# Optimization experiments

Measured on AMD Instinct MI355X. Metric: run time of the kernel, lower is better.

The kernel has to match this reference:

```python
import jax, jax.numpy as jnp
import numpy as np

B, C, D, H = 32, 512, 512, 8  # batch, enc_in channels, d_model, num_heads
W = D // H                    # per-head width in frequency domain
BN_EPS = 1e-5


def _lin(k, din, dout):
    # weight stored as [in, out]; apply as x @ W + b (equivalent to torch Linear)
    return jax.random.normal(k, (din, dout), jnp.float32) / np.sqrt(din)


def setup_inputs() -> dict:
    key = jax.random.key(0)
    ks = jax.random.split(key, 16)
    return {
        "x": jax.random.normal(ks[0], (B, C, D), jnp.float32),
        "W_in": _lin(ks[1], D, D), "b_in": jnp.zeros((D,), jnp.float32),
        "W_q": _lin(ks[2], D, D), "b_q": jnp.zeros((D,), jnp.float32),
        "W_k": _lin(ks[3], D, D), "b_k": jnp.zeros((D,), jnp.float32),
        "W_v": _lin(ks[4], D, D), "b_v": jnp.zeros((D,), jnp.float32),
        "temperature": jnp.ones((H, 1), jnp.float32),
        "W1a": _lin(ks[5], D, D), "b1a": jnp.zeros((D,), jnp.float32),
        "bn_gamma": jnp.ones((C,), jnp.float32),
        "bn_beta": jnp.zeros((C,), jnp.float32),
        "bn_mean": 0.1 * jax.random.normal(ks[6], (C,), jnp.float32),
        "bn_var": 1.0 + 0.1 * jax.random.uniform(ks[7], (C,), jnp.float32),
        "W1b": _lin(ks[8], D, D), "b1b": jnp.zeros((D,), jnp.float32),
        "W_out": _lin(ks[9], 2 * D, D), "b_out": jnp.zeros((D,), jnp.float32),
    }


def _complex_l2_normalize(z):
    # torch F.normalize on complex: divide by L2 norm of |z| along last dim
    n = jnp.sqrt(jnp.sum(jnp.abs(z) ** 2, axis=-1, keepdims=True))
    return z / jnp.maximum(n, 1e-12)


def reference(x, W_in, b_in, W_q, b_q, W_k, b_k, W_v, b_v, temperature,
              W1a, b1a, bn_gamma, bn_beta, bn_mean, bn_var, W1b, b1b,
              W_out, b_out):
    b, c, d = x.shape
    h, w = H, d // H

    conv2 = x @ W_in + b_in                       # in_projector (dropout = identity, eval)
    q = conv2 @ W_q + b_q
    k = conv2 @ W_k + b_k
    v = conv2 @ W_v + b_v

    # 2-D FFT over last two axes (c, d), as torch.fft.fft2 does on [b, c, d]
    q_f = jnp.fft.fft2(q).reshape(b, c, h, w)
    k_f = jnp.fft.fft2(k).reshape(b, c, h, w)
    v_f = jnp.fft.fft2(v).reshape(b, c, h, w)
    tep = jnp.fft.fft2(conv2)                     # [b, c, d] complex

    q_f = _complex_l2_normalize(q_f)
    k_f = _complex_l2_normalize(k_f)

    # [b, c, h, h] complex attention scores, scaled by real (8,1) temperature
    attn = jnp.einsum('bchw,bcgw->bchg', q_f, k_f) * temperature
    # custom complex softmax: softmax real and imag parts independently
    attn = jax.nn.softmax(attn.real, axis=-1) + 1j * jax.nn.softmax(attn.imag, axis=-1)

    out_f = jnp.einsum('bchg,bcgw->bchw', attn, v_f)        # complex [b,c,h,w]
    out_f = jnp.abs(jnp.fft.ifft2(out_f)).reshape(b, c, d)  # ifft2 over (h,w)

    # gated branch: Linear -> BatchNorm1d(enc_in, eval) -> ReLU -> Linear -> Sigmoid
    g = tep.real @ W1a + b1a
    g = (g - bn_mean[None, :, None]) * jax.lax.rsqrt(bn_var[None, :, None] + BN_EPS)
    g = g * bn_gamma[None, :, None] + bn_beta[None, :, None]
    g = jax.nn.relu(g) @ W1b + b1b
    g = jax.nn.sigmoid(g)
    out_l = jnp.abs(jnp.fft.ifft2(g * tep))                 # [b, c, d]

    out2 = jnp.concatenate([out_f, out_l], axis=-1) @ W_out + b_out
    return out2 + conv2
```

## Files before the change

### kernel.cpp

```cpp
#include <hip/hip_runtime.h>
#include <hip/hip_bf16.h>

#define FFT_PI 3.14159265358979323846f
#define FOFF(i) ((i) + ((i) >> 3))
#define PR(r) ((r) ^ (((r) >> 3) & 1))

typedef __hip_bfloat16 bf16;
typedef short bf8_t __attribute__((ext_vector_type(8)));
typedef float f4_t __attribute__((ext_vector_type(4)));

__device__ inline float bf2f(unsigned short u) {
    union { unsigned int i; float f; } v; v.i = ((unsigned int)u) << 16; return v.f;
}
__device__ inline unsigned short f2bf(float f) {
    bf16 h = __float2bfloat16(f);
    union { bf16 h; unsigned short u; } v; v.h = h; return v.u;
}
__device__ inline float2 c_load(const ushort2* p) {
    ushort2 u = *p;
    return make_float2(bf2f(u.x), bf2f(u.y));
}
__device__ inline ushort2 c_store(float2 z) {
    ushort2 u; u.x = f2bf(z.x); u.y = f2bf(z.y); return u;
}
__device__ inline int brev6(int t) {
    return ((t & 1) << 5) | ((t & 2) << 3) | ((t & 4) << 1) |
           ((t & 8) >> 1) | ((t & 16) >> 3) | ((t & 32) >> 5);
}
__device__ inline float2 cadd(float2 a, float2 b){ return make_float2(a.x+b.x, a.y+b.y); }
__device__ inline float2 csub(float2 a, float2 b){ return make_float2(a.x-b.x, a.y-b.y); }
__device__ inline float2 cmul(float2 a, float2 b){
    return make_float2(a.x*b.x - a.y*b.y, a.x*b.y + a.y*b.x);
}
__device__ inline float2 cmuli(float2 a, float s){ return make_float2(-s*a.y, s*a.x); }

__device__ inline float2 twd(const float2* TWL, int j, float sign) {
    float2 t = TWL[j];
    return make_float2(t.x, sign * t.y);
}

__device__ inline void async_load16(const void* gp, void* lp) {
    __builtin_amdgcn_global_load_lds(
        (const __attribute__((address_space(1))) void*)gp,
        (__attribute__((address_space(3))) void*)lp, 16, 0, 0);
}

__global__ __launch_bounds__(256) void transpose_cvt_all(
    const float* __restrict__ s0, const float* __restrict__ s1,
    const float* __restrict__ s2, const float* __restrict__ s3,
    const float* __restrict__ s4, const float* __restrict__ s5,
    const float* __restrict__ s6, bf16* __restrict__ Wt)
{
    const int z = blockIdx.z;
    const int R = (z == 6) ? 1024 : 512;
    if (blockIdx.y * 32 >= R) return;
    const float* src = (z == 0) ? s0 : (z == 1) ? s1 : (z == 2) ? s2 :
                       (z == 3) ? s3 : (z == 4) ? s4 : (z == 5) ? s5 : s6;
    bf16* dst = Wt + (long)z * 262144;
    const int C = 512;

    __shared__ float tile[32][33];
    const int bx = blockIdx.x * 32;
    const int by = blockIdx.y * 32;
    const int tx = threadIdx.x, ty = threadIdx.y;
#pragma unroll
    for (int i = 0; i < 32; i += 8)
        tile[ty + i][tx] = src[(long)(by + ty + i) * C + bx + tx];
    __syncthreads();
#pragma unroll
    for (int i = 0; i < 32; i += 8)
        dst[(long)(bx + ty + i) * R + by + tx] = __float2bfloat16(tile[tx][ty + i]);
}

__global__ __launch_bounds__(256) void mfma_gemm(
    const void* __restrict__ Av, const void* __restrict__ Av2,
    int a_type, int lda, int ksplit,
    const bf16* __restrict__ Bt, int ldb,
    const float* __restrict__ bias0, const float* __restrict__ bias1,
    const float* __restrict__ bias2,
    void* __restrict__ C0, void* __restrict__ C1, void* __restrict__ C2,
    int nper, int out_type, int ldc, int K,
    const float* __restrict__ e0, const float* __restrict__ e1,
    const float* __restrict__ e2, const float* __restrict__ e3)
{
    __shared__ short Asub[128 * 32];
    __shared__ short Bsub[128 * 32];

    const int tid = threadIdx.x;
    const int n0 = blockIdx.x * 128;
    const int m0 = blockIdx.y * 128;
    const int l  = tid & 63;
    const int wv = tid >> 6;
    const int wm = wv & 1, wn = wv >> 1;

    f4_t acc[4][4];
#pragma unroll
    for (int i = 0; i < 4; i++)
#pragma unroll
        for (int j = 0; j < 4; j++)
            acc[i][j] = (f4_t)0.f;

    const int crow = l >> 2;
    const int cpc  = (l & 3) * 8;

    for (int k0 = 0; k0 < K; k0 += 32) {
        const void* As = (k0 < ksplit) ? Av : Av2;
        const int kk = (k0 < ksplit) ? k0 : (k0 - ksplit);

        if (a_type == 0) {
#pragma unroll
            for (int c = 0; c < 2; c++) {
                const int chunk = wv * 2 + c;
                const int row = chunk * 16 + crow;
                async_load16((const bf16*)As + (long)(m0 + row) * lda + kk + cpc,
                             &Asub[chunk * 512]);
                async_load16(Bt + (long)(n0 + row) * ldb + k0 + cpc,
                             &Bsub[chunk * 512]);
            }
        } else {
            const int srow = tid >> 2;
            const int sc8  = (tid & 3) * 8;
#pragma unroll
            for (int p = 0; p < 2; p++) {
                const int row = srow + p * 64;
                const float4* src = (const float4*)((const float*)As
                    + (long)(m0 + row) * lda + kk + sc8);
                float4 u0 = src[0], u1 = src[1];
                bf8_t av;
                av[0] = (short)f2bf(u0.x); av[1] = (short)f2bf(u0.y);
                av[2] = (short)f2bf(u0.z); av[3] = (short)f2bf(u0.w);
                av[4] = (short)f2bf(u1.x); av[5] = (short)f2bf(u1.y);
                av[6] = (short)f2bf(u1.z); av[7] = (short)f2bf(u1.w);
                *(bf8_t*)&Asub[row * 32 + sc8] = av;
            }
#pragma unroll
            for (int c = 0; c < 2; c++) {
                const int chunk = wv * 2 + c;
                const int row = chunk * 16 + crow;
                async_load16(Bt + (long)(n0 + row) * ldb + k0 + cpc,
                             &Bsub[chunk * 512]);
            }
        }
        __syncthreads();

        bf8_t a_frag[4], b_frag[4];
        const int ko = (l >> 4) * 8;
        const int lr = l & 15;
#pragma unroll
        for (int fm = 0; fm < 4; fm++)
            a_frag[fm] = *(bf8_t*)&Asub[(wm * 64 + fm * 16 + lr) * 32 + ko];
#pragma unroll
        for (int fn = 0; fn < 4; fn++)
            b_frag[fn] = *(bf8_t*)&Bsub[(wn * 64 + fn * 16 + lr) * 32 + ko];
#pragma unroll
        for (int fm = 0; fm < 4; fm++)
#pragma unroll
            for (int fn = 0; fn < 4; fn++)
                acc[fm][fn] = __builtin_amdgcn_mfma_f32_16x16x32_bf16(
                    b_frag[fn], a_frag[fm], acc[fm][fn], 0, 0, 0);
        __syncthreads();
    }

    const int sel = n0 / nper;
    const int nb  = sel * nper;
    const float* biasl = (sel == 0) ? bias0 : ((sel == 1) ? bias1 : bias2);
    void* Cl = (sel == 0) ? C0 : ((sel == 1) ? C1 : C2);

    const int em = m0 + wm * 64 + (l & 15);
    const int en = n0 + wn * 64 + ((l >> 4) << 2);
#pragma unroll
    for (int fm = 0; fm < 4; fm++) {
        const long m = em + fm * 16;
        float bnm = 0.f, bnr = 1.f, bng = 1.f, bnb = 0.f;
        if (out_type == 3) {
            const int c = (int)(m & 511);
            bnm = e0[c];
            bnr = 1.0f / sqrtf(e1[c] + 1e-5f);
            bng = e2[c];
            bnb = e3[c];
        }
#pragma unroll
        for (int fn = 0; fn < 4; fn++) {
            const int n = en + fn * 16;
            const int nl = n - nb;
            f4_t v = acc[fm][fn];
            if (biasl) {
#pragma unroll
                for (int r = 0; r < 4; r++) v[r] += biasl[nl + r];
            }
            if (out_type == 0) {
                float4 o; o.x = v[0]; o.y = v[1]; o.z = v[2]; o.w = v[3];
                *(float4*)((float*)Cl + m * ldc + nl) = o;
            } else if (out_type == 1) {
                union { unsigned short u[4]; ushort4 q; } o;
#pragma unroll
                for (int r = 0; r < 4; r++) o.u[r] = f2bf(v[r]);
                *(ushort4*)((bf16*)Cl + m * ldc + nl) = o.q;
            } else if (out_type == 2) {
                union { ushort2 u2[4]; uint4 q; } o;
#pragma unroll
                for (int r = 0; r < 4; r++) { o.u2[r].x = f2bf(v[r]); o.u2[r].y = 0; }
                *(uint4*)((ushort2*)Cl + m * ldc + nl) = o.q;
            } else if (out_type == 3) {
                union { unsigned short u[4]; ushort4 q; } o;
#pragma unroll
                for (int r = 0; r < 4; r++)
                    o.u[r] = f2bf(fmaxf((v[r] - bnm) * bnr * bng + bnb, 0.f));
                *(ushort4*)((bf16*)Cl + m * ldc + nl) = o.q;
            } else {
                union { unsigned short u[4]; ushort4 q; } rsd;
                rsd.q = *(const ushort4*)((const unsigned short*)e0 + m * ldc + nl);
                float4 o;
                o.x = v[0] + bf2f(rsd.u[0]);
                o.y = v[1] + bf2f(rsd.u[1]);
                o.z = v[2] + bf2f(rsd.u[2]);
                o.w = v[3] + bf2f(rsd.u[3]);
                *(float4*)((float*)Cl + m * ldc + nl) = o;
            }
        }
    }
}

__device__ inline void dft8(float2* x, float sgn)
{
    const float c45 = 0.70710678118654752f;
    float2 e0, e1, e2, e3, o0, o1, o2, o3;
    {
        float2 u0 = cadd(x[0], x[4]), u1 = csub(x[0], x[4]);
        float2 u2 = cadd(x[2], x[6]), u3 = cmuli(csub(x[2], x[6]), sgn);
        e0 = cadd(u0, u2); e1 = cadd(u1, u3); e2 = csub(u0, u2); e3 = csub(u1, u3);
    }
    {
        float2 u0 = cadd(x[1], x[5]), u1 = csub(x[1], x[5]);
        float2 u2 = cadd(x[3], x[7]), u3 = cmuli(csub(x[3], x[7]), sgn);
        o0 = cadd(u0, u2); o1 = cadd(u1, u3); o2 = csub(u0, u2); o3 = csub(u1, u3);
    }
    const float2 w1 = make_float2(c45, sgn * c45);
    const float2 w3 = make_float2(-c45, sgn * c45);
    o1 = cmul(o1, w1);
    o2 = cmuli(o2, sgn);
    o3 = cmul(o3, w3);
    x[0] = cadd(e0, o0); x[4] = csub(e0, o0);
    x[1] = cadd(e1, o1); x[5] = csub(e1, o1);
    x[2] = cadd(e2, o2); x[6] = csub(e2, o2);
    x[3] = cadd(e3, o3); x[7] = csub(e3, o3);
}

__device__ inline void fft512_r8u(ushort2* bx0, ushort2* by0, int lane, float sign,
                                  const float2* TWL)
{
    ushort2* bx = bx0;
    ushort2* by = by0;
#pragma unroll
    for (int st = 0; st < 3; st++) {
        int n, m, sstr, p, q;
        if (st == 0)      { n = 512; m = 64; sstr = 1;  p = lane;      q = 0; }
        else if (st == 1) { n = 64;  m = 8;  sstr = 8;  p = lane >> 3; q = lane & 7; }
        else              { n = 8;   m = 1;  sstr = 64; p = 0;         q = lane; }
        float2 x[8];
#pragma unroll
        for (int r = 0; r < 8; r++) x[r] = c_load(&bx[FOFF(q + sstr * (p + r * m))]);
        dft8(x, sign);
        if (p) {
            const int step = (st == 0) ? 1 : 8;
#pragma unroll
            for (int k = 1; k < 8; k++)
                x[k] = cmul(x[k], twd(TWL, p * k * step, sign));
        }
#pragma unroll
        for (int k = 0; k < 8; k++) by[FOFF(q + sstr * (8 * p + k))] = c_store(x[k]);
        ushort2* t = bx; bx = by; by = t;
    }
}

__device__ inline void twl_fill(float2* TWL, int t, int nthreads)
{
    for (int j = t; j < 512; j += nthreads) {
        float sw, cw;
        __sincosf((2.0f * FFT_PI) * (float)j / 512.0f, &sw, &cw);
        TWL[j] = make_float2(cw, sw);
    }
}

__global__ __launch_bounds__(256) void fft8_rows_all(
    ushort2* __restrict__ qkv, const bf16* __restrict__ conv2,
    ushort2* __restrict__ tb)
{
    __shared__ ushort2 B0[4][576], B1[4][576];
    __shared__ float2 TWL[512];
    const int buf = blockIdx.x >> 12;
    const int lb  = blockIdx.x & 4095;
    const int li = threadIdx.x >> 6, lane = threadIdx.x & 63;
    const long line = (long)lb * 4 + li;
    twl_fill(TWL, threadIdx.x, 256);

    if (buf < 3) {
        ushort2* s = qkv + (long)buf * 8388608 + line * 512;
        uint4 r0 = *(const uint4*)(s + lane * 8);
        uint4 r1 = *(const uint4*)(s + lane * 8 + 4);
        ushort2* dst = &B0[li][9 * lane];
        const ushort2* pp = (const ushort2*)&r0;
#pragma unroll
        for (int j = 0; j < 4; j++) dst[j] = pp[j];
        pp = (const ushort2*)&r1;
#pragma unroll
        for (int j = 0; j < 4; j++) dst[4 + j] = pp[j];
        __syncthreads();
        fft512_r8u(B0[li], B1[li], lane, -1.f, TWL);
        ushort2* src = &B1[li][9 * lane];
        union { ushort2 u[4]; uint4 q; } o0, o1;
#pragma unroll
        for (int j = 0; j < 4; j++) o0.u[j] = src[j];
#pragma unroll
        for (int j = 0; j < 4; j++) o1.u[j] = src[4 + j];
        *(uint4*)(s + lane * 8) = o0.q;
        *(uint4*)(s + lane * 8 + 4) = o1.q;
    } else {
        uint4 raw = *(const uint4*)((const unsigned short*)conv2 + line * 512 + lane * 8);
        const unsigned short* pp = (const unsigned short*)&raw;
        ushort2* d = &B0[li][9 * lane];
#pragma unroll
        for (int j = 0; j < 8; j++) { ushort2 u; u.x = pp[j]; u.y = 0; d[j] = u; }
        __syncthreads();
        fft512_r8u(B0[li], B1[li], lane, -1.f, TWL);
        ushort2* s = tb + line * 512;
        ushort2* src = &B1[li][9 * lane];
        union { ushort2 u[4]; uint4 q; } o0, o1;
#pragma unroll
        for (int j = 0; j < 4; j++) o0.u[j] = src[j];
#pragma unroll
        for (int j = 0; j < 4; j++) o1.u[j] = src[4 + j];
        *(uint4*)(s + lane * 8) = o0.q;
        *(uint4*)(s + lane * 8 + 4) = o1.q;
    }
}

__global__ __launch_bounds__(256) void fft8_rows_gated(
    const bf16* __restrict__ g2, ushort2* __restrict__ tep)
{
    __shared__ ushort2 B0[4][576], B1[4][576];
    __shared__ float2 TWL[512];
    const int li = threadIdx.x >> 6, lane = threadIdx.x & 63;
    const long line = (long)blockIdx.x * 4 + li;
    ushort2* s = tep + line * 512;
    twl_fill(TWL, threadIdx.x, 256);
    {
        uint4 rg = *(const uint4*)((const unsigned short*)g2 + line * 512 + lane * 8);
        uint4 r0 = *(const uint4*)(s + lane * 8);
        uint4 r1 = *(const uint4*)(s + lane * 8 + 4);
        const unsigned short* gp = (const unsigned short*)&rg;
        ushort2* d = &B0[li][9 * lane];
        const ushort2* pp = (const ushort2*)&r0;
#pragma unroll
        for (int j = 0; j < 4; j++) {
            float sg = 1.0f / (1.0f + __expf(-bf2f(gp[j])));
            float2 z = c_load(pp + j);
            d[j] = c_store(make_float2(sg * z.x, sg * z.y));
        }
        pp = (const ushort2*)&r1;
#pragma unroll
        for (int j = 0; j < 4; j++) {
            float sg = 1.0f / (1.0f + __expf(-bf2f(gp[4 + j])));
            float2 z = c_load(pp + j);
            d[4 + j] = c_store(make_float2(sg * z.x, sg * z.y));
        }
    }
    __syncthreads();
    fft512_r8u(B0[li], B1[li], lane, +1.f, TWL);
    {
        const float sc = 1.0f / 512.0f;
        ushort2* src = &B1[li][9 * lane];
        union { ushort2 u[4]; uint4 q; } o0, o1;
#pragma unroll
        for (int j = 0; j < 4; j++) {
            float2 z = c_load(&src[j]);
            o0.u[j] = c_store(make_float2(z.x * sc, z.y * sc));
        }
#pragma unroll
        for (int j = 0; j < 4; j++) {
            float2 z = c_load(&src[4 + j]);
            o1.u[j] = c_store(make_float2(z.x * sc, z.y * sc));
        }
        *(uint4*)(s + lane * 8) = o0.q;
        *(uint4*)(s + lane * 8 + 4) = o1.q;
    }
}

__global__ __launch_bounds__(512) void fft8_cols16_c2c4(
    ushort2* __restrict__ data, bf16* __restrict__ tepReal, float sign)
{
    __shared__ __align__(16) ushort2 Bu[512][16];
    __shared__ float2 TWL[512];
    const int buf = blockIdx.x >> 10;
    const int rem = blockIdx.x & 1023;
    const int b   = rem >> 5;
    const int c0  = (rem & 31) * 16;
    ushort2* base = data + (long)buf * 8388608 + (long)b * 262144 + c0;
    const int t = threadIdx.x;
    const int lr = t >> 2;
    const int lq = t & 3;
    twl_fill(TWL, t, 512);

#pragma unroll
    for (int it = 0; it < 4; it++) {
        const int row = it * 128 + lr;
        uint4 raw = *(const uint4*)(base + (long)row * 512 + lq * 4);
        *(uint4*)&Bu[PR(row)][lq * 4] = raw;
    }
    __syncthreads();

    const int col = t & 15;
    const int rb  = t >> 4;
#pragma unroll
    for (int st = 0; st < 3; st++) {
        int n, m, s;
        if (st == 0)      { n = 512; m = 64; s = 1;  }
        else if (st == 1) { n = 64;  m = 8;  s = 8;  }
        else              { n = 8;   m = 1;  s = 64; }
        const int step = (st == 0) ? 1 : 8;
        float2 x[2][8];
        int ps[2], qs[2];
#pragma unroll
        for (int i = 0; i < 2; i++) {
            const int role = rb + 32 * i;
            int p, q;
            if (st == 0)      { p = role;      q = 0; }
            else if (st == 1) { p = role >> 3; q = role & 7; }
            else              { p = 0;         q = role; }
            ps[i] = p; qs[i] = q;
#pragma unroll
            for (int r = 0; r < 8; r++) {
                const int rr = q + s * (p + r * m);
                x[i][r] = c_load(&Bu[PR(rr)][col]);
            }
        }
        __syncthreads();
#pragma unroll
        for (int i = 0; i < 2; i++) {
            dft8(x[i], sign);
            const int p = ps[i];
            if (p) {
#pragma unroll
                for (int k = 1; k < 8; k++)
                    x[i][k] = cmul(x[i][k], twd(TWL, p * k * step, sign));
            }
#pragma unroll
            for (int k = 0; k < 8; k++) {
                const int rw = qs[i] + s * (8 * p + k);
                Bu[PR(rw)][col] = c_store(x[i][k]);
            }
        }
        __syncthreads();
    }

#pragma unroll
    for (int it = 0; it < 4; it++) {
        const int row = it * 128 + lr;
        union { uint4 q4; unsigned short s[8]; } o;
        o.q4 = *(const uint4*)&Bu[PR(row)][lq * 4];
        *(uint4*)(base + (long)row * 512 + lq * 4) = o.q4;
        if (buf == 3) {
            ushort4 rl;
            rl.x = o.s[0]; rl.y = o.s[2]; rl.z = o.s[4]; rl.w = o.s[6];
            *(ushort4*)(tepReal + (long)b * 262144 + (long)row * 512 + c0 + lq * 4) = rl;
        }
    }
}

__global__ __launch_bounds__(512) void fft8_cols16_abs(
    const ushort2* __restrict__ src, bf16* __restrict__ dst)
{
    __shared__ __align__(16) ushort2 Bu[512][16];
    __shared__ float2 TWL[512];
    const int b  = blockIdx.x >> 5;
    const int c0 = (blockIdx.x & 31) * 16;
    const ushort2* base = src + (long)b * 262144 + c0;
    const int t = threadIdx.x;
    const int lr = t >> 2;
    const int lq = t & 3;
    twl_fill(TWL, t, 512);

#pragma unroll
    for (int it = 0; it < 4; it++) {
        const int row = it * 128 + lr;
        uint4 raw = *(const uint4*)(base + (long)row * 512 + lq * 4);
        *(uint4*)&Bu[PR(row)][lq * 4] = raw;
    }
    __syncthreads();

    const int col = t & 15;
    const int rb  = t >> 4;
#pragma unroll
    for (int st = 0; st < 3; st++) {
        int n, m, s;
        if (st == 0)      { n = 512; m = 64; s = 1;  }
        else if (st == 1) { n = 64;  m = 8;  s = 8;  }
        else              { n = 8;   m = 1;  s = 64; }
        const int step = (st == 0) ? 1 : 8;
        float2 x[2][8];
        int ps[2], qs[2];
#pragma unroll
        for (int i = 0; i < 2; i++) {
            const int role = rb + 32 * i;
            int p, q;
            if (st == 0)      { p = role;      q = 0; }
            else if (st == 1) { p = role >> 3; q = role & 7; }
            else              { p = 0;         q = role; }
            ps[i] = p; qs[i] = q;
#pragma unroll
            for (int r = 0; r < 8; r++) {
                const int rr = q + s * (p + r * m);
                x[i][r] = c_load(&Bu[PR(rr)][col]);
            }
        }
        __syncthreads();
#pragma unroll
        for (int i = 0; i < 2; i++) {
            dft8(x[i], +1.f);
            const int p = ps[i];
            if (p) {
#pragma unroll
                for (int k = 1; k < 8; k++)
                    x[i][k] = cmul(x[i][k], twd(TWL, p * k * step, +1.f));
            }
#pragma unroll
            for (int k = 0; k < 8; k++) {
                const int rw = qs[i] + s * (8 * p + k);
                Bu[PR(rw)][col] = c_store(x[i][k]);
            }
        }
        __syncthreads();
    }

    const float sc = 1.0f / 512.0f;
#pragma unroll
    for (int it = 0; it < 4; it++) {
        const int row = it * 128 + lr;
        union { unsigned short u[4]; ushort4 q4; } o;
#pragma unroll
        for (int j = 0; j < 4; j++) {
            float2 z = c_load(&Bu[PR(row)][lq * 4 + j]);
            o.u[j] = f2bf(sqrtf(z.x * z.x + z.y * z.y) * sc);
        }
        *(ushort4*)(dst + (long)b * 262144 + (long)row * 512 + c0 + lq * 4) = o.q4;
    }
}

__global__ __launch_bounds__(256) void attn_kernel(
    const ushort2* __restrict__ qf, const ushort2* __restrict__ kf,
    const ushort2* __restrict__ vf, const float* __restrict__ temp,
    bf16* __restrict__ out_f)
{
    __shared__ ushort2 QS[4][8][68];
    __shared__ ushort2 KS[4][8][68];
    __shared__ float2 ATT[4][8][9];
    __shared__ float2 TW32[32];

    const int li = threadIdx.x >> 6, lane = threadIdx.x & 63;
    const int bc = blockIdx.x * 4 + li;
    const long base = (long)bc * 512;

    if (lane < 32) {
        float sw, cw;
        __sincosf((FFT_PI / 32.0f) * (float)lane, &sw, &cw);
        TW32[lane] = make_float2(cw, sw);
    }

    {
        const int h1 = lane >> 4, w1 = (lane & 15) * 4;
        uint4 q0 = *(const uint4*)(qf + base + lane * 4);
        uint4 q1 = *(const uint4*)(qf + base + 256 + lane * 4);
        uint4 k0 = *(const uint4*)(kf + base + lane * 4);
        uint4 k1 = *(const uint4*)(kf + base + 256 + lane * 4);
        *(uint4*)&QS[li][h1][w1]     = q0;
        *(uint4*)&QS[li][h1 + 4][w1] = q1;
        *(uint4*)&KS[li][h1][w1]     = k0;
        *(uint4*)&KS[li][h1 + 4][w1] = k1;
    }
    float2 v[8];
#pragma unroll
    for (int h = 0; h < 8; h++)
        v[h] = c_load(vf + base + h * 64 + lane);

    {
        const int h = lane >> 3, g = lane & 7;
        float ar = 0.f, ai = 0.f, nq = 0.f, nk = 0.f;
#pragma unroll
        for (int w = 0; w < 64; w += 4) {
            uint4 qa = *(const uint4*)&QS[li][h][w];
            uint4 kb = *(const uint4*)&KS[li][g][w];
            const unsigned short* qs = (const unsigned short*)&qa;
            const unsigned short* ks = (const unsigned short*)&kb;
#pragma unroll
            for (int j = 0; j < 4; j++) {
                float qx = bf2f(qs[2 * j]), qy = bf2f(qs[2 * j + 1]);
                float kx = bf2f(ks[2 * j]), ky = bf2f(ks[2 * j + 1]);
                ar += qx * kx - qy * ky;
                ai += qx * ky + qy * kx;
                nq += qx * qx + qy * qy;
                nk += kx * kx + ky * ky;
            }
        }
        const float iq = 1.0f / fmaxf(sqrtf(nq), 1e-12f);
        const float ik = 1.0f / fmaxf(sqrtf(nk), 1e-12f);
        const float s = temp[h] * iq * ik;
        ar *= s; ai *= s;
        float mr = ar, mi = ai;
#pragma unroll
        for (int o = 1; o < 8; o <<= 1) {
            mr = fmaxf(mr, __shfl_xor(mr, o, 64));
            mi = fmaxf(mi, __shfl_xor(mi, o, 64));
        }
        float er = __expf(ar - mr), ei = __expf(ai - mi);
        float sr = er, si = ei;
#pragma unroll
        for (int o = 1; o < 8; o <<= 1) {
            sr += __shfl_xor(sr, o, 64);
            si += __shfl_xor(si, o, 64);
        }
        ATT[li][h][g] = make_float2(er / sr, ei / si);
    }

    float2 o[8];
#pragma unroll
    for (int h = 0; h < 8; h++) {
        float orr = 0.f, oi = 0.f;
#pragma unroll
        for (int g = 0; g < 8; g++) {
            float2 a = ATT[li][h][g], b = v[g];
            orr += a.x * b.x - a.y * b.y;
            oi  += a.x * b.y + a.y * b.x;
        }
        o[h] = make_float2(orr, oi);
    }

#pragma unroll
    for (int m = 32; m >= 1; m >>= 1) {
        const int j = (lane & (m - 1)) * (32 / m);
        float2 wv = TW32[j];
        const float cw = wv.x, sw = wv.y;
        const bool low = (lane & m) == 0;
#pragma unroll
        for (int h = 0; h < 8; h++) {
            float px = __shfl_xor(o[h].x, m, 64);
            float py = __shfl_xor(o[h].y, m, 64);
            float nx, ny;
            if (low) {
                nx = o[h].x + px;
                ny = o[h].y + py;
            } else {
                float dx = px - o[h].x;
                float dy = py - o[h].y;
                nx = dx * cw - dy * sw;
                ny = dx * sw + dy * cw;
            }
            o[h].x = nx; o[h].y = ny;
        }
    }
    const int wr = brev6(lane);

    const float r2 = 0.70710678118654752f;
    const float W8x[8] = {1.f,  r2, 0.f, -r2, -1.f, -r2,  0.f,  r2};
    const float W8y[8] = {0.f,  r2, 1.f,  r2,  0.f, -r2, -1.f, -r2};
    unsigned short* stg = (unsigned short*)&QS[li][0][0];
#pragma unroll
    for (int kh = 0; kh < 8; kh++) {
        float sr = 0.f, si = 0.f;
#pragma unroll
        for (int n = 0; n < 8; n++) {
            const int idx = (n * kh) & 7;
            float wx = W8x[idx], wy = W8y[idx];
            sr += o[n].x * wx - o[n].y * wy;
            si += o[n].x * wy + o[n].y * wx;
        }
        stg[kh * 64 + wr] = f2bf(sqrtf(sr * sr + si * si) * (1.0f / 512.0f));
    }
    uint4 ov = *(uint4*)(stg + lane * 8);
    *(uint4*)((unsigned short*)out_f + base + lane * 8) = ov;
}

extern "C" void kernel_launch(void* const* d_in, const int* in_sizes, int n_in,
                              void* d_out, int out_size, void* d_ws, size_t ws_size,
                              hipStream_t stream)
{
    const float* x     = (const float*)d_in[0];
    const float* W_in  = (const float*)d_in[1];
    const float* b_in  = (const float*)d_in[2];
    const float* W_q   = (const float*)d_in[3];
    const float* b_q   = (const float*)d_in[4];
    const float* W_k   = (const float*)d_in[5];
    const float* b_k   = (const float*)d_in[6];
    const float* W_v   = (const float*)d_in[7];
    const float* b_v   = (const float*)d_in[8];
    const float* temp  = (const float*)d_in[9];
    const float* W1a   = (const float*)d_in[10];
    const float* b1a   = (const float*)d_in[11];
    const float* gam   = (const float*)d_in[12];
    const float* bet   = (const float*)d_in[13];
    const float* mea   = (const float*)d_in[14];
    const float* var   = (const float*)d_in[15];
    const float* W1b   = (const float*)d_in[16];
    const float* b1b   = (const float*)d_in[17];
    const float* W_out = (const float*)d_in[18];
    const float* b_out = (const float*)d_in[19];

    char* wsb = (char*)d_ws;
    const long MB = 1024 * 1024;
    bf16*    conv2b  = (bf16*)wsb;
    bf16*    tepReal = (bf16*)(wsb + 16 * MB);
    ushort2* Qb    = (ushort2*)(wsb + 32 * MB);
    ushort2* Kb    = (ushort2*)(wsb + 64 * MB);
    ushort2* Vb    = (ushort2*)(wsb + 96 * MB);
    ushort2* Tb    = (ushort2*)(wsb + 128 * MB);
    bf16*    Wt    = (bf16*)(wsb + 160 * MB);
    bf16* WT_in  = Wt;
    bf16* WT_q   = Wt + 262144;
    bf16* WT_1a  = Wt + 4 * 262144;
    bf16* WT_1b  = Wt + 5 * 262144;
    bf16* WT_out = Wt + 6 * 262144;
    bf16* outF = (bf16*)Qb;
    bf16* g1b  = (bf16*)Kb;
    bf16* outL = (bf16*)Kb;
    bf16* g2b  = (bf16*)Vb;

    const dim3 ggrid(4, 128), gblk(256);
    const int BIG = 1 << 30;
    const int RB = 4096;

    transpose_cvt_all<<<dim3(16, 32, 7), dim3(32, 8), 0, stream>>>(
        W_in, W_q, W_k, W_v, W1a, W1b, W_out, Wt);

    mfma_gemm<<<ggrid, gblk, 0, stream>>>(
        x, x, 1, 512, BIG, WT_in, 512, b_in, nullptr, nullptr,
        conv2b, nullptr, nullptr, BIG, 1, 512, 512,
        nullptr, nullptr, nullptr, nullptr);

    mfma_gemm<<<dim3(12, 128), gblk, 0, stream>>>(
        conv2b, conv2b, 0, 512, BIG, WT_q, 512, b_q, b_k, b_v,
        Qb, Kb, Vb, 512, 2, 512, 512,
        nullptr, nullptr, nullptr, nullptr);

    fft8_rows_all<<<4 * RB, 256, 0, stream>>>(Qb, conv2b, Tb);

    fft8_cols16_c2c4<<<4096, 512, 0, stream>>>(Qb, tepReal, -1.f);

    attn_kernel<<<RB, 256, 0, stream>>>(Qb, Kb, Vb, temp, outF);

    mfma_gemm<<<ggrid, gblk, 0, stream>>>(
        tepReal, tepReal, 0, 512, BIG, WT_1a, 512, b1a, nullptr, nullptr,
        g1b, nullptr, nullptr, BIG, 3, 512, 512,
        mea, var, gam, bet);

    mfma_gemm<<<ggrid, gblk, 0, stream>>>(
        g1b, g1b, 0, 512, BIG, WT_1b, 512, b1b, nullptr, nullptr,
        g2b, nullptr, nullptr, BIG, 1, 512, 512,
        nullptr, nullptr, nullptr, nullptr);

    fft8_rows_gated<<<RB, 256, 0, stream>>>(g2b, Tb);
    fft8_cols16_abs<<<1024, 512, 0, stream>>>(Tb, outL);

    mfma_gemm<<<ggrid, gblk, 0, stream>>>(
        outF, outL, 0, 512, 512, WT_out, 1024, b_out, nullptr, nullptr,
        d_out, nullptr, nullptr, BIG, 4, 512, 1024,
        (const float*)conv2b, nullptr, nullptr, nullptr);
}
```

Baseline: 519.8 us.

## Co-schedule attention blocks with gated-branch GEMMs and row FFT in fused launches

The attention kernel is split into three slices, and each slice is merged into the same launch as one gated-branch stage: the two GEMMs and the gated row FFT. Blocks are dispatched by block index to either body and share a union of shared memory. The aim is to let the independent attention work and the memory-heavy gated work overlap on the GPU and fill idle CUs. The gated intermediates move into the output buffer to avoid aliasing with Kb/Vb, which attention still reads. The cost is that the shared-memory union takes the larger of the two sizes, and register usage is now that of the heavier body, which may lower occupancy.

```diff
diff --git a/kernel.cpp b/kernel.cpp
--- a/kernel.cpp
+++ b/kernel.cpp
@@ -44,6 +44,22 @@
         (const __attribute__((address_space(1))) void*)gp,
         (__attribute__((address_space(3))) void*)lp, 16, 0, 0);
 }
+
+struct AttnSmem {
+    ushort2 QS[4][8][68];
+    ushort2 KS[4][8][68];
+    float2  ATT[4][8][9];
+    float2  TW32[32];
+};
+struct GemmSmem {
+    short Asub[128 * 32];
+    short Bsub[128 * 32];
+};
+struct RowsSmem {
+    ushort2 B0[4][576];
+    ushort2 B1[4][576];
+    float2  TWL[512];
+};
 
 __global__ __launch_bounds__(256) void transpose_cvt_all(
     const float* __restrict__ s0, const float* __restrict__ s1,
@@ -72,7 +88,7 @@
         dst[(long)(bx + ty + i) * R + by + tx] = __float2bfloat16(tile[tx][ty + i]);
 }
 
-__global__ __launch_bounds__(256) void mfma_gemm(
+__device__ void gemm_body(GemmSmem& sm, int bx, int by,
     const void* __restrict__ Av, const void* __restrict__ Av2,
     int a_type, int lda, int ksplit,
     const bf16* __restrict__ Bt, int ldb,
@@ -83,12 +99,12 @@
     const float* __restrict__ e0, const float* __restrict__ e1,
     const float* __restrict__ e2, const float* __restrict__ e3)
 {
-    __shared__ short Asub[128 * 32];
-    __shared__ short Bsub[128 * 32];
+    short* Asub = sm.Asub;
+    short* Bsub = sm.Bsub;
 
     const int tid = threadIdx.x;
-    const int n0 = blockIdx.x * 128;
-    const int m0 = blockIdx.y * 128;
+    const int n0 = bx * 128;
+    const int m0 = by * 128;
     const int l  = tid & 63;
     const int wv = tid >> 6;
     const int wm = wv & 1, wn = wv >> 1;
@@ -221,6 +237,23 @@
     }
 }
 
+__global__ __launch_bounds__(256) void mfma_gemm(
+    const void* __restrict__ Av, const void* __restrict__ Av2,
+    int a_type, int lda, int ksplit,
+    const bf16* __restrict__ Bt, int ldb,
+    const float* __restrict__ bias0, const float* __restrict__ bias1,
+    const float* __restrict__ bias2,
+    void* __restrict__ C0, void* __restrict__ C1, void* __restrict__ C2,
+    int nper, int out_type, int ldc, int K,
+    const float* __restrict__ e0, const float* __restrict__ e1,
+    const float* __restrict__ e2, const float* __restrict__ e3)
+{
+    __shared__ GemmSmem sm;
+    gemm_body(sm, blockIdx.x, blockIdx.y, Av, Av2, a_type, lda, ksplit,
+              Bt, ldb, bias0, bias1, bias2, C0, C1, C2,
+              nper, out_type, ldc, K, e0, e1, e2, e3);
+}
+
 __device__ inline void dft8(float2* x, float sgn)
 {
     const float c45 = 0.70710678118654752f;
@@ -335,21 +368,19 @@
     }
 }
 
-__global__ __launch_bounds__(256) void fft8_rows_gated(
+__device__ void rows_gated_body(RowsSmem& sm, int blk,
     const bf16* __restrict__ g2, ushort2* __restrict__ tep)
 {
-    __shared__ ushort2 B0[4][576], B1[4][576];
-    __shared__ float2 TWL[512];
     const int li = threadIdx.x >> 6, lane = threadIdx.x & 63;
-    const long line = (long)blockIdx.x * 4 + li;
+    const long line = (long)blk * 4 + li;
     ushort2* s = tep + line * 512;
-    twl_fill(TWL, threadIdx.x, 256);
+    twl_fill(sm.TWL, threadIdx.x, 256);
     {
         uint4 rg = *(const uint4*)((const unsigned short*)g2 + line * 512 + lane * 8);
         uint4 r0 = *(const uint4*)(s + lane * 8);
         uint4 r1 = *(const uint4*)(s + lane * 8 + 4);
         const unsigned short* gp = (const unsigned short*)&rg;
-        ushort2* d = &B0[li][9 * lane];
+        ushort2* d = &sm.B0[li][9 * lane];
         const ushort2* pp = (const ushort2*)&r0;
 #pragma unroll
         for (int j = 0; j < 4; j++) {
@@ -366,10 +397,10 @@
         }
     }
     __syncthreads();
-    fft512_r8u(B0[li], B1[li], lane, +1.f, TWL);
+    fft512_r8u(sm.B0[li], sm.B1[li], lane, +1.f, sm.TWL);
     {
         const float sc = 1.0f / 512.0f;
-        ushort2* src = &B1[li][9 * lane];
+        ushort2* src = &sm.B1[li][9 * lane];
         union { ushort2 u[4]; uint4 q; } o0, o1;
 #pragma unroll
         for (int j = 0; j < 4; j++) {
@@ -546,24 +577,19 @@
     }
 }
 
-__global__ __launch_bounds__(256) void attn_kernel(
+__device__ void attn_body(AttnSmem& sm, int blk,
     const ushort2* __restrict__ qf, const ushort2* __restrict__ kf,
     const ushort2* __restrict__ vf, const float* __restrict__ temp,
     bf16* __restrict__ out_f)
 {
-    __shared__ ushort2 QS[4][8][68];
-    __shared__ ushort2 KS[4][8][68];
-    __shared__ float2 ATT[4][8][9];
-    __shared__ float2 TW32[32];
-
     const int li = threadIdx.x >> 6, lane = threadIdx.x & 63;
-    const int bc = blockIdx.x * 4 + li;
+    const int bc = blk * 4 + li;
     const long base = (long)bc * 512;
 
     if (lane < 32) {
         float sw, cw;
         __sincosf((FFT_PI / 32.0f) * (float)lane, &sw, &cw);
-        TW32[lane] = make_float2(cw, sw);
+        sm.TW32[lane] = make_float2(cw, sw);
     }
 
     {
@@ -572,10 +598,10 @@
         uint4 q1 = *(const uint4*)(qf + base + 256 + lane * 4);
         uint4 k0 = *(const uint4*)(kf + base + lane * 4);
         uint4 k1 = *(const uint4*)(kf + base + 256 + lane * 4);
-        *(uint4*)&QS[li][h1][w1]     = q0;
-        *(uint4*)&QS[li][h1 + 4][w1] = q1;
-        *(uint4*)&KS[li][h1][w1]     = k0;
-        *(uint4*)&KS[li][h1 + 4][w1] = k1;
+        *(uint4*)&sm.QS[li][h1][w1]     = q0;
+        *(uint4*)&sm.QS[li][h1 + 4][w1] = q1;
+        *(uint4*)&sm.KS[li][h1][w1]     = k0;
+        *(uint4*)&sm.KS[li][h1 + 4][w1] = k1;
     }
     float2 v[8];
 #pragma unroll
@@ -587,8 +613,8 @@
         float ar = 0.f, ai = 0.f, nq = 0.f, nk = 0.f;
 #pragma unroll
         for (int w = 0; w < 64; w += 4) {
-            uint4 qa = *(const uint4*)&QS[li][h][w];
-            uint4 kb = *(const uint4*)&KS[li][g][w];
+            uint4 qa = *(const uint4*)&sm.QS[li][h][w];
+            uint4 kb = *(const uint4*)&sm.KS[li][g][w];
             const unsigned short* qs = (const unsigned short*)&qa;
             const unsigned short* ks = (const unsigned short*)&kb;
 #pragma unroll
@@ -618,7 +644,7 @@
             sr += __shfl_xor(sr, o, 64);
             si += __shfl_xor(si, o, 64);
         }
-        ATT[li][h][g] = make_float2(er / sr, ei / si);
+        sm.ATT[li][h][g] = make_float2(er / sr, ei / si);
     }
 
     float2 o[8];
@@ -627,7 +653,7 @@
         float orr = 0.f, oi = 0.f;
 #pragma unroll
         for (int g = 0; g < 8; g++) {
-            float2 a = ATT[li][h][g], b = v[g];
+            float2 a = sm.ATT[li][h][g], b = v[g];
             orr += a.x * b.x - a.y * b.y;
             oi  += a.x * b.y + a.y * b.x;
         }
@@ -637,7 +663,7 @@
 #pragma unroll
     for (int m = 32; m >= 1; m >>= 1) {
         const int j = (lane & (m - 1)) * (32 / m);
-        float2 wv = TW32[j];
+        float2 wv = sm.TW32[j];
         const float cw = wv.x, sw = wv.y;
         const bool low = (lane & m) == 0;
 #pragma unroll
@@ -662,7 +688,7 @@
     const float r2 = 0.70710678118654752f;
     const float W8x[8] = {1.f,  r2, 0.f, -r2, -1.f, -r2,  0.f,  r2};
     const float W8y[8] = {0.f,  r2, 1.f,  r2,  0.f, -r2, -1.f, -r2};
-    unsigned short* stg = (unsigned short*)&QS[li][0][0];
+    unsigned short* stg = (unsigned short*)&sm.QS[li][0][0];
 #pragma unroll
     for (int kh = 0; kh < 8; kh++) {
         float sr = 0.f, si = 0.f;
@@ -677,6 +703,50 @@
     }
     uint4 ov = *(uint4*)(stg + lane * 8);
     *(uint4*)((unsigned short*)out_f + base + lane * 8) = ov;
+}
+
+__global__ __launch_bounds__(256) void fused_attn_gemm(
+    int nattn, int abase,
+    const ushort2* __restrict__ qf, const ushort2* __restrict__ kf,
+    const ushort2* __restrict__ vf, const float* __restrict__ temp,
+    bf16* __restrict__ out_f,
+    const void* __restrict__ Av, const bf16* __restrict__ Bt,
+    const float* __restrict__ bias0, void* __restrict__ C0,
+    int out_type,
+    const float* __restrict__ e0, const float* __restrict__ e1,
+    const float* __restrict__ e2, const float* __restrict__ e3)
+{
+    __shared__ __align__(16) unsigned char smraw[
+        sizeof(AttnSmem) > sizeof(GemmSmem) ? sizeof(AttnSmem) : sizeof(GemmSmem)];
+    const int bid = blockIdx.x;
+    if (bid < nattn) {
+        attn_body(*reinterpret_cast<AttnSmem*>(smraw), abase + bid,
+                  qf, kf, vf, temp, out_f);
+    } else {
+        const int g = bid - nattn;
+        gemm_body(*reinterpret_cast<GemmSmem*>(smraw), g & 3, g >> 2,
+                  Av, Av, 0, 512, 1 << 30, Bt, 512,
+                  bias0, nullptr, nullptr, C0, nullptr, nullptr,
+                  1 << 30, out_type, 512, 512, e0, e1, e2, e3);
+    }
+}
+
+__global__ __launch_bounds__(256) void fused_attn_rowsg(
+    int nattn, int abase,
+    const ushort2* __restrict__ qf, const ushort2* __restrict__ kf,
+    const ushort2* __restrict__ vf, const float* __restrict__ temp,
+    bf16* __restrict__ out_f,
+    const bf16* __restrict__ g2, ushort2* __restrict__ tep)
+{
+    __shared__ __align__(16) unsigned char smraw[
+        sizeof(AttnSmem) > sizeof(RowsSmem) ? sizeof(AttnSmem) : sizeof(RowsSmem)];
+    const int bid = blockIdx.x;
+    if (bid < nattn) {
+        attn_body(*reinterpret_cast<AttnSmem*>(smraw), abase + bid,
+                  qf, kf, vf, temp, out_f);
+    } else {
+        rows_gated_body(*reinterpret_cast<RowsSmem*>(smraw), bid - nattn, g2, tep);
+    }
 }
 
 extern "C" void kernel_launch(void* const* d_in, const int* in_sizes, int n_in,
@@ -719,9 +789,9 @@
     bf16* WT_1b  = Wt + 5 * 262144;
     bf16* WT_out = Wt + 6 * 262144;
     bf16* outF = (bf16*)Qb;
-    bf16* g1b  = (bf16*)Kb;
+    bf16* g1b  = (bf16*)d_out;
+    bf16* g2b  = (bf16*)d_out + 8388608;
     bf16* outL = (bf16*)Kb;
-    bf16* g2b  = (bf16*)Vb;
 
     const dim3 ggrid(4, 128), gblk(256);
     const int BIG = 1 << 30;
@@ -744,19 +814,17 @@
 
     fft8_cols16_c2c4<<<4096, 512, 0, stream>>>(Qb, tepReal, -1.f);
 
-    attn_kernel<<<RB, 256, 0, stream>>>(Qb, Kb, Vb, temp, outF);
-
-    mfma_gemm<<<ggrid, gblk, 0, stream>>>(
-        tepReal, tepReal, 0, 512, BIG, WT_1a, 512, b1a, nullptr, nullptr,
-        g1b, nullptr, nullptr, BIG, 3, 512, 512,
-        mea, var, gam, bet);
-
-    mfma_gemm<<<ggrid, gblk, 0, stream>>>(
-        g1b, g1b, 0, 512, BIG, WT_1b, 512, b1b, nullptr, nullptr,
-        g2b, nullptr, nullptr, BIG, 1, 512, 512,
-        nullptr, nullptr, nullptr, nullptr);
-
-    fft8_rows_gated<<<RB, 256, 0, stream>>>(g2b, Tb);
+    fused_attn_gemm<<<1365 + 512, gblk, 0, stream>>>(
+        1365, 0, Qb, Kb, Vb, temp, outF,
+        tepReal, WT_1a, b1a, g1b, 3, mea, var, gam, bet);
+
+    fused_attn_gemm<<<1365 + 512, gblk, 0, stream>>>(
+        1365, 1365, Qb, Kb, Vb, temp, outF,
+        g1b, WT_1b, b1b, g2b, 1, nullptr, nullptr, nullptr, nullptr);
+
+    fused_attn_rowsg<<<1366 + RB, gblk, 0, stream>>>(
+        1366, 2730, Qb, Kb, Vb, temp, outF, g2b, Tb);
+
     fft8_cols16_abs<<<1024, 512, 0, stream>>>(Tb, outL);
 
     mfma_gemm<<<ggrid, gblk, 0, stream>>>(
```

New measurement: 772.4 us. +48.6%, slower.
